# Optimization experiments

Hardware: AMD Instinct MI355X
Metric: run time of the kernel (lower is better)

The kernel has to match this reference:

```python
import jax, jax.numpy as jnp
import numpy as np
from jax import lax

K = 8          # num_classes
C_IN = 256     # in_channels
EPS = 1e-5


def resize_bilinear_ac(x, H, W):
    """Bilinear resize with align_corners=True. x: [B,C,h,w] -> [B,C,H,W]."""
    B, C, h, w = x.shape
    if h == H and w == W:
        return x
    ys = jnp.linspace(0.0, h - 1.0, H)
    xs = jnp.linspace(0.0, w - 1.0, W)
    y0 = jnp.floor(ys).astype(jnp.int32)
    x0 = jnp.floor(xs).astype(jnp.int32)
    y1 = jnp.minimum(y0 + 1, h - 1)
    x1 = jnp.minimum(x0 + 1, w - 1)
    wy = (ys - y0.astype(x.dtype))[None, None, :, None]
    wx = (xs - x0.astype(x.dtype))[None, None, None, :]
    g00 = x[:, :, y0][:, :, :, x0]
    g01 = x[:, :, y0][:, :, :, x1]
    g10 = x[:, :, y1][:, :, :, x0]
    g11 = x[:, :, y1][:, :, :, x1]
    top = g00 * (1.0 - wx) + g01 * wx
    bot = g10 * (1.0 - wx) + g11 * wx
    return top * (1.0 - wy) + bot * wy


def setup_inputs() -> dict:
    key = jax.random.key(0)
    ks = jax.random.split(key, 16)
    shapes = [(2, 256, 128, 128), (2, 256, 64, 64), (2, 256, 32, 32), (2, 256, 16, 16), (2, 256, 8, 8)]
    inp = {}
    for i, s in enumerate(shapes):
        inp[f"feat{i}"] = jax.random.normal(ks[i], s, dtype=jnp.float32)
    inp["attr_feat"] = jax.random.normal(ks[5], (2, K * C_IN, 64, 64), dtype=jnp.float32)
    # learned params
    inp["mlp_f_w"] = jax.random.normal(ks[6], (256, 256), dtype=jnp.float32) * 0.02
    inp["mlp_f_b"] = jnp.zeros((256,), dtype=jnp.float32)
    inp["mlp_a_w"] = jax.random.normal(ks[7], (256, 256), dtype=jnp.float32) * 0.02
    inp["mlp_a_b"] = jnp.zeros((256,), dtype=jnp.float32)
    # 5 grouped convs: [out=2048, in_per_group=256, 3, 3] each, no bias (BN follows)
    inp["conv_w"] = jax.random.normal(ks[8], (5, K * C_IN, C_IN, 3, 3), dtype=jnp.float32) * 0.02
    inp["bn_gamma"] = jnp.ones((5, K * C_IN), dtype=jnp.float32)
    inp["bn_beta"] = jnp.zeros((5, K * C_IN), dtype=jnp.float32)
    inp["bn_mean"] = jax.random.normal(ks[9], (5, K * C_IN), dtype=jnp.float32) * 0.1
    inp["bn_var"] = jax.random.uniform(ks[10], (5, K * C_IN), dtype=jnp.float32, minval=0.5, maxval=1.5)
    return inp


def _forward(feats, attr_feat, mlp_f_w, mlp_f_b, mlp_a_w, mlp_a_b, conv_w, bn_gamma, bn_beta, bn_mean, bn_var):
    B = attr_feat.shape[0]
    # global avg pool attr -> [B, K, C] -> mlp_a
    avg_attr = attr_feat.mean(axis=(2, 3)).reshape(B, K, C_IN)
    avg_attr = avg_attr @ mlp_a_w.T + mlp_a_b  # [B,K,256]
    outs = []
    for i, x in enumerate(feats):
        _, C, H, W = x.shape
        avg_x = x.mean(axis=(2, 3)) @ mlp_f_w.T + mlp_f_b          # [B,256]
        logits = jnp.einsum('bkc,bc->bk', avg_attr, avg_x)          # [B,K]
        attn = jax.nn.softmax(logits, axis=-1)
        y = resize_bilinear_ac(attr_feat, H, W)                      # [B,2048,H,W]
        y = lax.conv_general_dilated(
            y, conv_w[i], window_strides=(1, 1), padding=((1, 1), (1, 1)),
            dimension_numbers=('NCHW', 'OIHW', 'NCHW'), feature_group_count=K)
        inv = lax.rsqrt(bn_var[i] + EPS)
        y = (y - bn_mean[i][None, :, None, None]) * (inv * bn_gamma[i])[None, :, None, None] + bn_beta[i][None, :, None, None]
        y = jax.nn.relu(y)
        y = y.reshape(B, K, C, H, W)
        y = jnp.einsum('bkchw,bk->bchw', y, attn)                   # weighted sum over classes
        outs.append(jax.nn.relu(x + y))
    return tuple(outs)


def reference(feat0, feat1, feat2, feat3, feat4, attr_feat, mlp_f_w, mlp_f_b, mlp_a_w, mlp_a_b, conv_w, bn_gamma, bn_beta, bn_mean, bn_var):
    feats = [feat0, feat1, feat2, feat3, feat4]
    return _forward(feats, attr_feat, mlp_f_w, mlp_f_b, mlp_a_w, mlp_a_b, conv_w, bn_gamma, bn_beta, bn_mean, bn_var)
```

## Files before the change

### kernel.cpp

```cpp
#include <hip/hip_runtime.h>
#include <hip/hip_bf16.h>
#include <cstdint>

typedef __attribute__((ext_vector_type(8))) short short8;
typedef __attribute__((ext_vector_type(4))) float f32x4;

#define EPSV 1e-5f

__device__ __forceinline__ void gload_lds16(const void* g, void* l) {
  __builtin_amdgcn_global_load_lds(
      (const __attribute__((address_space(1))) void*)(uintptr_t)g,
      (__attribute__((address_space(3))) void*)(uint32_t)(uintptr_t)l,
      16, 0, 0);
}

__device__ __forceinline__ uint32_t f2bf_rne(float v) {
  const uint32_t u = __float_as_uint(v);
  const uint32_t r = ((u >> 16) & 1u) + 0x7fffu;
  return (u + r) >> 16;
}
__device__ __forceinline__ float bf2f(uint32_t u) {
  return __uint_as_float(u << 16);
}

__global__ void mean_kernel(const float* __restrict__ in, float* __restrict__ out,
                            int HW, float inv) {
  const int ch = blockIdx.x;
  const int t = threadIdx.x;
  const float* p = in + (size_t)ch * HW;
  float s = 0.f;
  const int nv = HW >> 2;
  const float4* pv = (const float4*)p;
  for (int i = t; i < nv; i += 256) { float4 v = pv[i]; s += v.x + v.y + v.z + v.w; }
  __shared__ float red[256];
  red[t] = s; __syncthreads();
  for (int off = 128; off > 0; off >>= 1) {
    if (t < off) red[t] += red[t + off];
    __syncthreads();
  }
  if (t == 0) out[ch] = red[0] * inv;
}

__global__ void meanf_kernel(const float* __restrict__ f0, const float* __restrict__ f1,
                             const float* __restrict__ f2, const float* __restrict__ f3,
                             const float* __restrict__ f4, float* __restrict__ out) {
  const int scale = blockIdx.x >> 9;
  const int ch = blockIdx.x & 511;
  const int t = threadIdx.x;
  const float* base;
  int HW;
  switch (scale) {
    case 0: base = f0; HW = 16384; break;
    case 1: base = f1; HW = 4096;  break;
    case 2: base = f2; HW = 1024;  break;
    case 3: base = f3; HW = 256;   break;
    default: base = f4; HW = 64;   break;
  }
  const float* p = base + (size_t)ch * HW;
  float s = 0.f;
  const int nv = HW >> 2;
  const float4* pv = (const float4*)p;
  for (int i = t; i < nv; i += 256) { float4 v = pv[i]; s += v.x + v.y + v.z + v.w; }
  __shared__ float red[256];
  red[t] = s; __syncthreads();
  for (int off = 128; off > 0; off >>= 1) {
    if (t < off) red[t] += red[t + off];
    __syncthreads();
  }
  if (t == 0) out[scale * 512 + ch] = red[0] / (float)HW;
}

__global__ void wtrans_kernel(const float* __restrict__ cw,
                              const float* __restrict__ gamma, const float* __restrict__ beta,
                              const float* __restrict__ mean, const float* __restrict__ var,
                              __hip_bfloat16* __restrict__ wt, float* __restrict__ bias) {
  __shared__ float wl[2304];
  const int oc = blockIdx.x;
  const int i  = blockIdx.y;
  const int t  = threadIdx.x;
  const int idx = i * 2048 + oc;
  const float* src = cw + (size_t)idx * 2304;
  for (int e = t; e < 2304; e += 256) wl[e] = src[e];
  __syncthreads();
  const float sc = rsqrtf(var[idx] + EPSV) * gamma[idx];
  if (t == 0) bias[idx] = beta[idx] - mean[idx] * sc;
  const int g = oc >> 8, co = oc & 255;
  const size_t dbase = (size_t)(i * 8 + g) * 9 * 65536 + co * 256 + t;
#pragma unroll
  for (int tap = 0; tap < 9; ++tap)
    wt[dbase + (size_t)tap * 65536] = __float2bfloat16(wl[t * 9 + tap] * sc);
}

__global__ void gate_kernel(const float* __restrict__ meanA, const float* __restrict__ meanF,
                            const float* __restrict__ Wa, const float* __restrict__ ba,
                            const float* __restrict__ Wf, const float* __restrict__ bfp,
                            float* __restrict__ attn) {
  __shared__ float mA[16 * 256];
  __shared__ float mF[10 * 256];
  __shared__ float pA[16 * 256];
  __shared__ float pF[10 * 256];
  __shared__ float lg[80];
  const int t = threadIdx.x;
  for (int i = t; i < 4096; i += 256) mA[i] = meanA[i];
  for (int i = t; i < 2560; i += 256) mF[i] = meanF[i];
  __syncthreads();
  {
    float acc[16];
#pragma unroll
    for (int j = 0; j < 16; ++j) acc[j] = 0.f;
    for (int ci = 0; ci < 256; ++ci) {
      const float w = Wa[t * 256 + ci];
#pragma unroll
      for (int j = 0; j < 16; ++j) acc[j] += mA[j * 256 + ci] * w;
    }
    const float bb = ba[t];
#pragma unroll
    for (int j = 0; j < 16; ++j) pA[j * 256 + t] = acc[j] + bb;
  }
  {
    float acc[10];
#pragma unroll
    for (int j = 0; j < 10; ++j) acc[j] = 0.f;
    for (int ci = 0; ci < 256; ++ci) {
      const float w = Wf[t * 256 + ci];
#pragma unroll
      for (int j = 0; j < 10; ++j) acc[j] += mF[j * 256 + ci] * w;
    }
    const float bb = bfp[t];
#pragma unroll
    for (int j = 0; j < 10; ++j) pF[j * 256 + t] = acc[j] + bb;
  }
  __syncthreads();
  if (t < 80) {
    const int i = t >> 4, r = t & 15, b = r >> 3, k = r & 7;
    const float* a = &pA[(b * 8 + k) * 256];
    const float* f = &pF[(i * 2 + b) * 256];
    float d = 0.f;
    for (int c = 0; c < 256; ++c) d += a[c] * f[c];
    lg[t] = d;
  }
  __syncthreads();
  if (t < 10) {
    const int base = t * 8;
    float m = lg[base];
    for (int k = 1; k < 8; ++k) m = fmaxf(m, lg[base + k]);
    float e[8], s = 0.f;
    for (int k = 0; k < 8; ++k) { e[k] = __expf(lg[base + k] - m); s += e[k]; }
    const float invs = 1.f / s;
    for (int k = 0; k < 8; ++k) attn[base + k] = e[k] * invs;
  }
}

__global__ void resize_kernel(const float* __restrict__ attr,
                              __hip_bfloat16* __restrict__ R,
                              int W, int Hp, int Wp, float scl) {
  const int bk = blockIdx.x;
  const int yp = blockIdx.y;
  const int t  = threadIdx.x;
  const size_t rowbase = ((size_t)bk * Hp + yp) * (size_t)Wp * 256;
  if (yp == 0 || yp == Hp - 1) {
    uint32_t* p = (uint32_t*)(R + rowbase);
    const int n = Wp * 128;
    for (int idx = t; idx < n; idx += 256) p[idx] = 0u;
    return;
  }
  const int y = yp - 1;
  const float fy = y * scl;
  int y0 = (int)floorf(fy); if (y0 > 63) y0 = 63;
  const float wy = fy - (float)y0;
  const int y1 = min(y0 + 1, 63);
  __shared__ float buf[2][64][65];
  const int cc = t >> 2, seg = (t & 3) * 16;
  const int bb = bk >> 3, k = bk & 7;
  const float* ab = attr + (size_t)bb * 2048 * 4096;
  const int ci = t & 63;
  for (int cq = 0; cq < 4; ++cq) {
    __syncthreads();
    {
      const int ch = k * 256 + cq * 64 + cc;
      const float* r0 = ab + ((size_t)ch * 64 + y0) * 64;
      const float* r1 = ab + ((size_t)ch * 64 + y1) * 64;
#pragma unroll
      for (int u = 0; u < 4; ++u) {
        float4 v0 = ((const float4*)r0)[(t & 3) * 4 + u];
        float4 v1 = ((const float4*)r1)[(t & 3) * 4 + u];
        buf[0][cc][seg + u * 4 + 0] = v0.x; buf[0][cc][seg + u * 4 + 1] = v0.y;
        buf[0][cc][seg + u * 4 + 2] = v0.z; buf[0][cc][seg + u * 4 + 3] = v0.w;
        buf[1][cc][seg + u * 4 + 0] = v1.x; buf[1][cc][seg + u * 4 + 1] = v1.y;
        buf[1][cc][seg + u * 4 + 2] = v1.z; buf[1][cc][seg + u * 4 + 3] = v1.w;
      }
    }
    __syncthreads();
    for (int x = t >> 6; x < W; x += 4) {
      const float fx = x * scl;
      int x0 = (int)floorf(fx); if (x0 > 63) x0 = 63;
      const float wx = fx - (float)x0;
      const int x1 = min(x0 + 1, 63);
      const float top = buf[0][ci][x0] * (1.f - wx) + buf[0][ci][x1] * wx;
      const float bot = buf[1][ci][x0] * (1.f - wx) + buf[1][ci][x1] * wx;
      R[rowbase + (size_t)(x + 1) * 256 + cq * 64 + ci] = __float2bfloat16(top * (1.f - wy) + bot * wy);
    }
    if (t < 64) {
      R[rowbase + cq * 64 + t] = __float2bfloat16(0.f);
      R[rowbase + (size_t)(Wp - 1) * 256 + cq * 64 + t] = __float2bfloat16(0.f);
    }
  }
}

__device__ __forceinline__ void coords36(int u, int g0, int& g, int& ty, int& tx, int& cq) {
  g = g0 + u / 36;
  const int r = u % 36;
  const int tap = r >> 2;
  cq = r & 3;
  ty = tap / 3;
  tx = tap - ty * 3;
}

__global__ __launch_bounds__(512, 1)
void conv256_kernel(const __hip_bfloat16* __restrict__ R,
                    const __hip_bfloat16* __restrict__ Wt,
                    const float* __restrict__ bias,
                    const float* __restrict__ attn,
                    __hip_bfloat16* __restrict__ zout,
                    int W, int lw, int Hp, int Wp, int HW,
                    int NB, int gcount) {
  __shared__ alignas(16) __hip_bfloat16 ldsA[2][256 * 64];
  __shared__ alignas(16) __hip_bfloat16 ldsB[2][256 * 64];
  const int tid  = threadIdx.x;
  const int lane = tid & 63;
  const int wave = __builtin_amdgcn_readfirstlane(tid >> 6);
  const int wm = (wave >> 2) * 128;
  const int wn = (wave & 3) * 64;

  const int X = gridDim.x;
  int xp = blockIdx.x, yv = blockIdx.y;
  if (X * gridDim.y == 256) {
    const int lin2 = blockIdx.x + X * blockIdx.y;
    const int d = (lin2 & 7) * 32 + (lin2 >> 3);
    yv = d / X; xp = d - yv * X;
  }
  const int n0 = xp * 256;
  const int bb = yv % NB;
  const int gs = yv / NB;
  const int g0 = gs * gcount;

  const int c8 = lane & 7, r8 = lane >> 3;
  const int sc = (c8 ^ r8) << 3;
  const int aoff0 = ((wave * 32 + r8) << 8) + sc;
  const int dst0  = wave * 2048;
  int boff[4];
#pragma unroll
  for (int q = 0; q < 4; ++q) {
    const int row = wave * 32 + q * 8 + r8;
    const int sg = n0 + row;
    const int y = sg >> lw, x = sg & (W - 1);
    boff[q] = ((y * Wp + x) << 8) + sc;
  }

  const size_t rgstride = (size_t)Hp * Wp * 256;
  const __hip_bfloat16* Rb = R + (size_t)bb * 8 * rgstride;

  const f32x4 fz = {0.f, 0.f, 0.f, 0.f};
  f32x4 acc[8][4];
  uint32_t finp[8][4][2];
#pragma unroll
  for (int mf = 0; mf < 8; ++mf)
#pragma unroll
    for (int nf = 0; nf < 4; ++nf) {
      acc[mf][nf] = fz; finp[mf][nf][0] = 0u; finp[mf][nf][1] = 0u;
    }

  const int nk = gcount * 36;
  {
    const __hip_bfloat16* wp = Wt + ((size_t)g0 * 9 << 16);
    const __hip_bfloat16* rp = Rb + (size_t)g0 * rgstride;
#pragma unroll
    for (int q = 0; q < 4; ++q) gload_lds16(wp + aoff0 + q * 2048, &ldsA[0][dst0 + q * 512]);
#pragma unroll
    for (int q = 0; q < 4; ++q) gload_lds16(rp + boff[q], &ldsB[0][dst0 + q * 512]);
  }

  int foldc = 0, gcur = g0;
  for (int t = 0; t < nk; ++t) {
    const int c = t & 1;
    const bool pf = (t + 1 < nk);
    int g1, ty1, tx1, cq1;
    coords36(pf ? t + 1 : t, g0, g1, ty1, tx1, cq1);
    const __hip_bfloat16* wp1 = Wt + (((size_t)g1 * 9 + ty1 * 3 + tx1) << 16) + (cq1 << 6);
    const __hip_bfloat16* rp1 = Rb + (size_t)g1 * rgstride + ((ty1 * Wp + tx1) << 8) + (cq1 << 6);

    asm volatile("s_waitcnt vmcnt(0)" ::: "memory");
    __builtin_amdgcn_s_barrier();
    asm volatile("" ::: "memory");

    const __hip_bfloat16* pA = &ldsA[c][0];
    const __hip_bfloat16* pB = &ldsB[c][0];
    __hip_bfloat16* dA = &ldsA[c ^ 1][0];
    __hip_bfloat16* dB = &ldsB[c ^ 1][0];

#pragma unroll
    for (int ks = 0; ks < 2; ++ks) {
      const int cb = ks * 4 + (lane >> 4);
      short8 bfv[4];
#pragma unroll
      for (int nf = 0; nf < 4; ++nf) {
        const int row = wn + nf * 16 + (lane & 15);
        bfv[nf] = *(const short8*)&pB[(row << 6) + ((cb ^ (row & 7)) << 3)];
      }
#pragma unroll
      for (int h = 0; h < 2; ++h) {
        short8 af[4];
#pragma unroll
        for (int m = 0; m < 4; ++m) {
          const int row = wm + (h * 4 + m) * 16 + (lane & 15);
          af[m] = *(const short8*)&pA[(row << 6) + ((cb ^ (row & 7)) << 3)];
        }
        if (ks == 0 && pf) {
          if (h == 0) {
#pragma unroll
            for (int q = 0; q < 4; ++q) gload_lds16(wp1 + aoff0 + q * 2048, dA + dst0 + q * 512);
          } else {
#pragma unroll
            for (int q = 0; q < 4; ++q) gload_lds16(rp1 + boff[q], dB + dst0 + q * 512);
          }
        }
        __builtin_amdgcn_s_barrier();
        __builtin_amdgcn_sched_barrier(0);
        __builtin_amdgcn_s_setprio(1);
#pragma unroll
        for (int m = 0; m < 4; ++m)
#pragma unroll
          for (int nf = 0; nf < 4; ++nf)
            acc[h * 4 + m][nf] = __builtin_amdgcn_mfma_f32_16x16x32_bf16(
                af[m], bfv[nf], acc[h * 4 + m][nf], 0, 0, 0);
        __builtin_amdgcn_s_setprio(0);
        __builtin_amdgcn_s_barrier();
        asm volatile("" ::: "memory");
      }
    }

    if (++foldc == 36) {
      foldc = 0;
      const float aw = attn[bb * 8 + gcur];
#pragma unroll
      for (int mf = 0; mf < 8; ++mf) {
        const int cobase = wm + mf * 16 + ((lane >> 4) << 2);
#pragma unroll
        for (int pr = 0; pr < 2; ++pr) {
          const float b0v = bias[(gcur << 8) + cobase + pr * 2 + 0];
          const float b1v = bias[(gcur << 8) + cobase + pr * 2 + 1];
#pragma unroll
          for (int nf = 0; nf < 4; ++nf) {
            const uint32_t p = finp[mf][nf][pr];
            const float f0 = __uint_as_float(p << 16)
                           + aw * fmaxf(acc[mf][nf][pr * 2 + 0] + b0v, 0.f);
            const float f1 = __uint_as_float(p & 0xffff0000u)
                           + aw * fmaxf(acc[mf][nf][pr * 2 + 1] + b1v, 0.f);
            finp[mf][nf][pr] = (f2bf_rne(f1) << 16) | f2bf_rne(f0);
          }
        }
#pragma unroll
        for (int nf = 0; nf < 4; ++nf) acc[mf][nf] = fz;
      }
      ++gcur;
    }
  }

  __hip_bfloat16* zb = zout + (size_t)(gs * 2 + bb) * 256 * (size_t)HW;
#pragma unroll
  for (int mf = 0; mf < 8; ++mf) {
    const int cobase = wm + mf * 16 + ((lane >> 4) << 2);
#pragma unroll
    for (int nf = 0; nf < 4; ++nf) {
      const int n = n0 + wn + nf * 16 + (lane & 15);
#pragma unroll
      for (int pr = 0; pr < 2; ++pr) {
        const uint32_t p = finp[mf][nf][pr];
        zb[(size_t)(cobase + pr * 2 + 0) * HW + n] =
            __float2bfloat16(__uint_as_float(p << 16));
        zb[(size_t)(cobase + pr * 2 + 1) * HW + n] =
            __float2bfloat16(__uint_as_float(p & 0xffff0000u));
      }
    }
  }
}

__global__ __launch_bounds__(256, 2)
void conv_kernel(const __hip_bfloat16* __restrict__ R,
                 const __hip_bfloat16* __restrict__ Wt,
                 const float* __restrict__ bias,
                 const float* __restrict__ attn,
                 const float* __restrict__ featp,
                 void* __restrict__ outp,
                 int W, int lw, int Hp, int Wp, int HW,
                 int b0, int NB, int gcount) {
  __shared__ alignas(16) __hip_bfloat16 ldsA[2][128 * 64];
  __shared__ alignas(16) __hip_bfloat16 ldsB[3][128 * 64];
  const int tid  = threadIdx.x;
  const int lane = tid & 63;
  const int wave = __builtin_amdgcn_readfirstlane(tid >> 6);
  const int wm = (wave >> 1) * 64;
  const int wn = (wave & 1) * 64;

  const int nx  = gridDim.x;
  const int lin = blockIdx.x;
  const int pos = ((nx & 7) == 0) ? ((lin & 7) * (nx >> 3) + (lin >> 3)) : lin;
  const int co0 = (pos & 1) * 128;
  const int n0  = (pos >> 1) * 128;

  const int bb  = (int)blockIdx.y % NB;
  const int gs  = (int)blockIdx.y / NB;
  const int b   = b0 + bb;
  const int g0  = gs * gcount;

  const int c8 = lane & 7;
  const int r8 = lane >> 3;
  int aoff[4], boff[4], dst[4];
#pragma unroll
  for (int q = 0; q < 4; ++q) {
    const int row = (wave * 4 + q) * 8 + r8;
    const int sc = (c8 ^ (row & 7)) << 3;
    aoff[q] = ((co0 + row) << 8) + sc;
    int sg = n0 + row; if (sg >= HW) sg = HW - 1;
    const int y = sg >> lw, x = sg & (W - 1);
    boff[q] = ((y * Wp + x) << 8) + sc;
    dst[q] = (wave * 4 + q) * 512;
  }

  const size_t rgstride = (size_t)Hp * Wp * 256;
  const __hip_bfloat16* Rb = R + (size_t)bb * 8 * rgstride;

  const f32x4 fz = {0.f, 0.f, 0.f, 0.f};
  f32x4 fin[4][4], acc[4][4];
#pragma unroll
  for (int mf = 0; mf < 4; ++mf)
#pragma unroll
    for (int nf = 0; nf < 4; ++nf) { fin[mf][nf] = fz; acc[mf][nf] = fz; }

  const int nstages = gcount * 36;
  {
    int g, ty, tx, cq;
    coords36(0, g0, g, ty, tx, cq);
    const __hip_bfloat16* wp = Wt + (((size_t)g * 9 + ty * 3 + tx) << 16) + (cq << 6);
    const __hip_bfloat16* rp = Rb + (size_t)g * rgstride + ((ty * Wp + tx) << 8) + (cq << 6);
#pragma unroll
    for (int q = 0; q < 4; ++q) gload_lds16(wp + aoff[q], &ldsA[0][dst[q]]);
#pragma unroll
    for (int q = 0; q < 4; ++q) gload_lds16(rp + boff[q], &ldsB[0][dst[q]]);
    coords36(1 < nstages ? 1 : 0, g0, g, ty, tx, cq);
    const __hip_bfloat16* rp1 = Rb + (size_t)g * rgstride + ((ty * Wp + tx) << 8) + (cq << 6);
#pragma unroll
    for (int q = 0; q < 4; ++q) gload_lds16(rp1 + boff[q], &ldsB[1][dst[q]]);
  }

  int bcur = 0, b2 = 2;
  int foldc = 0, gcur = g0;

  for (int s = 0; s < nstages; ++s) {
    __builtin_amdgcn_s_barrier();
    asm volatile("" ::: "memory");
    if (s + 1 < nstages) {
      int g, ty, tx, cq;
      coords36(s + 1, g0, g, ty, tx, cq);
      const __hip_bfloat16* wp = Wt + (((size_t)g * 9 + ty * 3 + tx) << 16) + (cq << 6);
      __hip_bfloat16* dA = &ldsA[(s + 1) & 1][0];
#pragma unroll
      for (int q = 0; q < 4; ++q) gload_lds16(wp + aoff[q], dA + dst[q]);
    }
    if (s + 2 < nstages) {
      int g, ty, tx, cq;
      coords36(s + 2, g0, g, ty, tx, cq);
      const __hip_bfloat16* rp = Rb + (size_t)g * rgstride + ((ty * Wp + tx) << 8) + (cq << 6);
      __hip_bfloat16* dB = &ldsB[b2][0];
#pragma unroll
      for (int q = 0; q < 4; ++q) gload_lds16(rp + boff[q], dB + dst[q]);
    }
    if (s + 2 < nstages)      asm volatile("s_waitcnt vmcnt(12)" ::: "memory");
    else if (s + 1 < nstages) asm volatile("s_waitcnt vmcnt(8)" ::: "memory");
    else                      asm volatile("s_waitcnt vmcnt(0)" ::: "memory");
    __builtin_amdgcn_s_barrier();
    asm volatile("" ::: "memory");

    const __hip_bfloat16* pA = &ldsA[s & 1][0];
    const __hip_bfloat16* pB = &ldsB[bcur][0];
#pragma unroll
    for (int ks = 0; ks < 2; ++ks) {
      short8 af[4], bfv[4];
      const int cb = ks * 4 + (lane >> 4);
#pragma unroll
      for (int mf = 0; mf < 4; ++mf) {
        const int row = wm + mf * 16 + (lane & 15);
        af[mf] = *(const short8*)&pA[(row << 6) + ((cb ^ (row & 7)) << 3)];
      }
#pragma unroll
      for (int nf = 0; nf < 4; ++nf) {
        const int row = wn + nf * 16 + (lane & 15);
        bfv[nf] = *(const short8*)&pB[(row << 6) + ((cb ^ (row & 7)) << 3)];
      }
#pragma unroll
      for (int mf = 0; mf < 4; ++mf)
#pragma unroll
        for (int nf = 0; nf < 4; ++nf)
          acc[mf][nf] = __builtin_amdgcn_mfma_f32_16x16x32_bf16(
              af[mf], bfv[nf], acc[mf][nf], 0, 0, 0);
    }

    if (++bcur == 3) bcur = 0;
    if (++b2 == 3) b2 = 0;

    if (++foldc == 36) {
      foldc = 0;
      const float aw = attn[b * 8 + gcur];
#pragma unroll
      for (int mf = 0; mf < 4; ++mf) {
        const int cobase = co0 + wm + mf * 16 + ((lane >> 4) << 2);
#pragma unroll
        for (int r = 0; r < 4; ++r) {
          const float bs = bias[(gcur << 8) + cobase + r];
#pragma unroll
          for (int nf = 0; nf < 4; ++nf) {
            fin[mf][nf][r] += aw * fmaxf(acc[mf][nf][r] + bs, 0.f);
            acc[mf][nf][r] = 0.f;
          }
        }
      }
      ++gcur;
    }
  }

  const size_t plane = (size_t)256 * HW;
  if (featp) {
    const float* fb = featp + (size_t)b * plane;
    float* ob = (float*)outp + (size_t)b * plane;
#pragma unroll
    for (int mf = 0; mf < 4; ++mf) {
      const int cobase = co0 + wm + mf * 16 + ((lane >> 4) << 2);
#pragma unroll
      for (int nf = 0; nf < 4; ++nf) {
        const int n = n0 + wn + nf * 16 + (lane & 15);
        if (n < HW) {
#pragma unroll
          for (int r = 0; r < 4; ++r) {
            const size_t idx = (size_t)(cobase + r) * HW + n;
            ob[idx] = fmaxf(fb[idx] + fin[mf][nf][r], 0.f);
          }
        }
      }
    }
  } else {
    __hip_bfloat16* zb = (__hip_bfloat16*)outp + ((size_t)gs * 2 + b) * plane;
#pragma unroll
    for (int mf = 0; mf < 4; ++mf) {
      const int cobase = co0 + wm + mf * 16 + ((lane >> 4) << 2);
#pragma unroll
      for (int nf = 0; nf < 4; ++nf) {
        const int n = n0 + wn + nf * 16 + (lane & 15);
        if (n < HW) {
#pragma unroll
          for (int r = 0; r < 4; ++r)
            zb[(size_t)(cobase + r) * HW + n] = __float2bfloat16(fin[mf][nf][r]);
        }
      }
    }
  }
}

__global__ void reduce_kernel(const __hip_bfloat16* __restrict__ z,
                              const float* __restrict__ feat,
                              float* __restrict__ outp, int total, int S) {
  const int i4 = (blockIdx.x * 256 + threadIdx.x) * 4;
  if (i4 >= total) return;
  float4 f = *(const float4*)(feat + i4);
  float s0 = f.x, s1 = f.y, s2 = f.z, s3 = f.w;
  for (int j = 0; j < S; ++j) {
    const ushort4 v = *(const ushort4*)(z + (size_t)j * total + i4);
    s0 += bf2f(v.x);
    s1 += bf2f(v.y);
    s2 += bf2f(v.z);
    s3 += bf2f(v.w);
  }
  float4 o = {fmaxf(s0, 0.f), fmaxf(s1, 0.f), fmaxf(s2, 0.f), fmaxf(s3, 0.f)};
  *(float4*)(outp + i4) = o;
}

extern "C" void kernel_launch(void* const* d_in, const int* in_sizes, int n_in,
                              void* d_out, int out_size, void* d_ws, size_t ws_size,
                              hipStream_t stream) {
  const float* feat[5];
  for (int i = 0; i < 5; ++i) feat[i] = (const float*)d_in[i];
  const float* attr = (const float*)d_in[5];
  const float* mfw = (const float*)d_in[6];
  const float* mfb = (const float*)d_in[7];
  const float* maw = (const float*)d_in[8];
  const float* mab = (const float*)d_in[9];
  const float* cw  = (const float*)d_in[10];
  const float* bng = (const float*)d_in[11];
  const float* bnb = (const float*)d_in[12];
  const float* bnm = (const float*)d_in[13];
  const float* bnv = (const float*)d_in[14];
  float* out = (float*)d_out;

  char* ws = (char*)d_ws;
  float* attnW = (float*)(ws);
  float* meanA = (float*)(ws + 512);
  float* meanF = (float*)(ws + 20480);
  float* biasW = (float*)(ws + 32768);
  __hip_bfloat16* Wt = (__hip_bfloat16*)(ws + 131072);
  const size_t R_OFF = 47316992;
  __hip_bfloat16* Rbuf = (__hip_bfloat16*)(ws + R_OFF);

  const bool full = ws_size >= (size_t)219316224;
  const int NB = full ? 2 : 1;
  __hip_bfloat16* zbuf = (__hip_bfloat16*)(ws + R_OFF + (size_t)NB * 69222400);

  static const int HS[5] = {128, 64, 32, 16, 8};
  static const size_t OOFF[5] = {0, 8388608, 10485760, 11010048, 11141120};

  mean_kernel<<<4096, 256, 0, stream>>>(attr, meanA, 4096, 1.f / 4096.f);
  meanf_kernel<<<2560, 256, 0, stream>>>(feat[0], feat[1], feat[2], feat[3], feat[4], meanF);
  wtrans_kernel<<<dim3(2048, 5), 256, 0, stream>>>(cw, bng, bnb, bnm, bnv, Wt, biasW);
  gate_kernel<<<1, 256, 0, stream>>>(meanA, meanF, maw, mab, mfw, mfb, attnW);

  for (int i = 0; i < 5; ++i) {
    const int H = HS[i], W = H, HW = H * W, Hp = H + 2, Wp = W + 2;
    const int lw = 31 - __builtin_clz((unsigned)W);
    const float scl = 63.f / (float)(H - 1);

    if (full) {
      resize_kernel<<<dim3(16, Hp), 256, 0, stream>>>(attr, Rbuf, W, Hp, Wp, scl);
      if (i <= 1) {
        const int S = (i == 0) ? 2 : 8;
        const int gcount = 8 / S;
        conv256_kernel<<<dim3(HW / 256, 2 * S), 512, 0, stream>>>(
            Rbuf, Wt + (size_t)i * 8 * 9 * 65536, biasW + i * 2048, attnW + i * 16,
            zbuf, W, lw, Hp, Wp, HW, 2, gcount);
        const int total = 2 * 256 * HW;
        reduce_kernel<<<(total / 4 + 255) / 256, 256, 0, stream>>>(
            zbuf, feat[i], out + OOFF[i], total, S);
      } else {
        const int ntiles = (HW + 127) / 128;
        conv_kernel<<<dim3(ntiles * 2, 2 * 8), 256, 0, stream>>>(
            Rbuf, Wt + (size_t)i * 8 * 9 * 65536, biasW + i * 2048, attnW + i * 16,
            nullptr, zbuf, W, lw, Hp, Wp, HW, 0, 2, 1);
        const int total = 2 * 256 * HW;
        reduce_kernel<<<(total / 4 + 255) / 256, 256, 0, stream>>>(
            zbuf, feat[i], out + OOFF[i], total, 8);
      }
    } else {
      const int ntiles = (HW + 127) / 128;
      for (int b0 = 0; b0 < 2; ++b0) {
        resize_kernel<<<dim3(8, Hp), 256, 0, stream>>>(
            attr + (size_t)b0 * 2048 * 4096, Rbuf, W, Hp, Wp, scl);
        conv_kernel<<<dim3(ntiles * 2, 1), 256, 0, stream>>>(
            Rbuf, Wt + (size_t)i * 8 * 9 * 65536, biasW + i * 2048, attnW + i * 16,
            feat[i], out + OOFF[i], W, lw, Hp, Wp, HW, b0, 1, 8);
      }
    }
  }
}
```

Before: 724.8 us.

## Reuse 64x64 bf16 padded resize as source for other scales, per-scale weight transform

Processes scale 1 (64x64, same size as attr) first, storing a padded bf16 NHWC copy of attr. The other scales then bilinearly resample from that compact bf16 buffer instead of re-reading the fp32 NCHW attr tensor, which cuts global traffic for the resize kernels. Weight transform now runs per scale into a single reused buffer, shrinking the workspace. The trade-off is extra bf16 rounding: the resized values are interpolated from already-rounded bf16 values, so they carry slightly more error.

Result: faster. 706.6 us, median of 2 (-2.5%).

```diff
diff --git a/kernel.cpp b/kernel.cpp
--- a/kernel.cpp
+++ b/kernel.cpp
@@ -73,10 +73,10 @@
 __global__ void wtrans_kernel(const float* __restrict__ cw,
                               const float* __restrict__ gamma, const float* __restrict__ beta,
                               const float* __restrict__ mean, const float* __restrict__ var,
-                              __hip_bfloat16* __restrict__ wt, float* __restrict__ bias) {
+                              __hip_bfloat16* __restrict__ wt, float* __restrict__ bias,
+                              int i) {
   __shared__ float wl[2304];
   const int oc = blockIdx.x;
-  const int i  = blockIdx.y;
   const int t  = threadIdx.x;
   const int idx = i * 2048 + oc;
   const float* src = cw + (size_t)idx * 2304;
@@ -85,7 +85,7 @@
   const float sc = rsqrtf(var[idx] + EPSV) * gamma[idx];
   if (t == 0) bias[idx] = beta[idx] - mean[idx] * sc;
   const int g = oc >> 8, co = oc & 255;
-  const size_t dbase = (size_t)(i * 8 + g) * 9 * 65536 + co * 256 + t;
+  const size_t dbase = (size_t)g * 9 * 65536 + co * 256 + t;
 #pragma unroll
   for (int tap = 0; tap < 9; ++tap)
     wt[dbase + (size_t)tap * 65536] = __float2bfloat16(wl[t * 9 + tap] * sc);
@@ -207,6 +207,60 @@
   }
 }
 
+__global__ void resizeR1_kernel(const __hip_bfloat16* __restrict__ R1,
+                                __hip_bfloat16* __restrict__ R,
+                                int W, int Hp, int Wp, float scl) {
+  const int bk = blockIdx.x;
+  const int yp = blockIdx.y;
+  const int t  = threadIdx.x;
+  const size_t rowbase = ((size_t)bk * Hp + yp) * (size_t)Wp * 256;
+  if (yp == 0 || yp == Hp - 1) {
+    uint32_t* p = (uint32_t*)(R + rowbase);
+    const int n = Wp * 128;
+    for (int idx = t; idx < n; idx += 256) p[idx] = 0u;
+    return;
+  }
+  const int y = yp - 1;
+  const float fy = y * scl;
+  int y0 = (int)floorf(fy); if (y0 > 63) y0 = 63;
+  const float wy = fy - (float)y0;
+  const int y1 = min(y0 + 1, 63);
+  const __hip_bfloat16* r0 = R1 + ((size_t)bk * 66 + (y0 + 1)) * 66 * 256 + 256;
+  const __hip_bfloat16* r1 = R1 + ((size_t)bk * 66 + (y1 + 1)) * 66 * 256 + 256;
+  const int ci4 = (t & 63) * 4;
+  for (int x = t >> 6; x < W; x += 4) {
+    const float fx = x * scl;
+    int x0 = (int)floorf(fx); if (x0 > 63) x0 = 63;
+    const float wx = fx - (float)x0;
+    const int x1 = min(x0 + 1, 63);
+    const ushort4 a00 = *(const ushort4*)&r0[x0 * 256 + ci4];
+    const ushort4 a01 = *(const ushort4*)&r0[x1 * 256 + ci4];
+    const ushort4 a10 = *(const ushort4*)&r1[x0 * 256 + ci4];
+    const ushort4 a11 = *(const ushort4*)&r1[x1 * 256 + ci4];
+    short4 st;
+    {
+      const float t0 = bf2f(a00.x) * (1.f - wx) + bf2f(a01.x) * wx;
+      const float b0 = bf2f(a10.x) * (1.f - wx) + bf2f(a11.x) * wx;
+      st.x = (short)f2bf_rne(t0 * (1.f - wy) + b0 * wy);
+      const float t1 = bf2f(a00.y) * (1.f - wx) + bf2f(a01.y) * wx;
+      const float b1 = bf2f(a10.y) * (1.f - wx) + bf2f(a11.y) * wx;
+      st.y = (short)f2bf_rne(t1 * (1.f - wy) + b1 * wy);
+      const float t2 = bf2f(a00.z) * (1.f - wx) + bf2f(a01.z) * wx;
+      const float b2 = bf2f(a10.z) * (1.f - wx) + bf2f(a11.z) * wx;
+      st.z = (short)f2bf_rne(t2 * (1.f - wy) + b2 * wy);
+      const float t3 = bf2f(a00.w) * (1.f - wx) + bf2f(a01.w) * wx;
+      const float b3 = bf2f(a10.w) * (1.f - wx) + bf2f(a11.w) * wx;
+      st.w = (short)f2bf_rne(t3 * (1.f - wy) + b3 * wy);
+    }
+    *(short4*)&R[rowbase + (size_t)(x + 1) * 256 + ci4] = st;
+  }
+  if (t < 64) {
+    const short4 z4 = {0, 0, 0, 0};
+    *(short4*)&R[rowbase + t * 4] = z4;
+    *(short4*)&R[rowbase + (size_t)(Wp - 1) * 256 + t * 4] = z4;
+  }
+}
+
 __device__ __forceinline__ void coords36(int u, int g0, int& g, int& ty, int& tx, int& cq) {
   g = g0 + u / 36;
   const int r = u % 36;
@@ -605,54 +659,67 @@
   float* meanA = (float*)(ws + 512);
   float* meanF = (float*)(ws + 20480);
   float* biasW = (float*)(ws + 32768);
-  __hip_bfloat16* Wt = (__hip_bfloat16*)(ws + 131072);
-  const size_t R_OFF = 47316992;
-  __hip_bfloat16* Rbuf = (__hip_bfloat16*)(ws + R_OFF);
-
-  const bool full = ws_size >= (size_t)219316224;
-  const int NB = full ? 2 : 1;
-  __hip_bfloat16* zbuf = (__hip_bfloat16*)(ws + R_OFF + (size_t)NB * 69222400);
+  __hip_bfloat16* Wt  = (__hip_bfloat16*)(ws + 131072);
+  __hip_bfloat16* R1  = (__hip_bfloat16*)(ws + 9568256);
+  __hip_bfloat16* R0  = (__hip_bfloat16*)(ws + 45252608);
+  __hip_bfloat16* zbuf = (__hip_bfloat16*)(ws + 183697408);
+
+  const bool full = ws_size >= (size_t)217251840;
 
   static const int HS[5] = {128, 64, 32, 16, 8};
   static const size_t OOFF[5] = {0, 8388608, 10485760, 11010048, 11141120};
+  static const int ORDER[5] = {1, 0, 2, 3, 4};
 
   mean_kernel<<<4096, 256, 0, stream>>>(attr, meanA, 4096, 1.f / 4096.f);
   meanf_kernel<<<2560, 256, 0, stream>>>(feat[0], feat[1], feat[2], feat[3], feat[4], meanF);
-  wtrans_kernel<<<dim3(2048, 5), 256, 0, stream>>>(cw, bng, bnb, bnm, bnv, Wt, biasW);
   gate_kernel<<<1, 256, 0, stream>>>(meanA, meanF, maw, mab, mfw, mfb, attnW);
 
-  for (int i = 0; i < 5; ++i) {
-    const int H = HS[i], W = H, HW = H * W, Hp = H + 2, Wp = W + 2;
-    const int lw = 31 - __builtin_clz((unsigned)W);
-    const float scl = 63.f / (float)(H - 1);
-
-    if (full) {
-      resize_kernel<<<dim3(16, Hp), 256, 0, stream>>>(attr, Rbuf, W, Hp, Wp, scl);
+  if (full) {
+    for (int oi = 0; oi < 5; ++oi) {
+      const int i = ORDER[oi];
+      const int H = HS[i], W = H, HW = H * W, Hp = H + 2, Wp = W + 2;
+      const int lw = 31 - __builtin_clz((unsigned)W);
+      const float scl = 63.f / (float)(H - 1);
+      __hip_bfloat16* Ri = (i == 1) ? R1 : R0;
+
+      wtrans_kernel<<<2048, 256, 0, stream>>>(cw, bng, bnb, bnm, bnv, Wt, biasW, i);
+      if (i == 1)
+        resize_kernel<<<dim3(16, Hp), 256, 0, stream>>>(attr, R1, W, Hp, Wp, scl);
+      else
+        resizeR1_kernel<<<dim3(16, Hp), 256, 0, stream>>>(R1, Ri, W, Hp, Wp, scl);
+
       if (i <= 1) {
         const int S = (i == 0) ? 2 : 8;
         const int gcount = 8 / S;
         conv256_kernel<<<dim3(HW / 256, 2 * S), 512, 0, stream>>>(
-            Rbuf, Wt + (size_t)i * 8 * 9 * 65536, biasW + i * 2048, attnW + i * 16,
+            Ri, Wt, biasW + i * 2048, attnW + i * 16,
             zbuf, W, lw, Hp, Wp, HW, 2, gcount);
         const int total = 2 * 256 * HW;
         reduce_kernel<<<(total / 4 + 255) / 256, 256, 0, stream>>>(
             zbuf, feat[i], out + OOFF[i], total, S);
       } else {
         const int ntiles = (HW + 127) / 128;
-        conv_kernel<<<dim3(ntiles * 2, 2 * 8), 256, 0, stream>>>(
-            Rbuf, Wt + (size_t)i * 8 * 9 * 65536, biasW + i * 2048, attnW + i * 16,
+        conv_kernel<<<dim3(ntiles * 2, 16), 256, 0, stream>>>(
+            Ri, Wt, biasW + i * 2048, attnW + i * 16,
             nullptr, zbuf, W, lw, Hp, Wp, HW, 0, 2, 1);
         const int total = 2 * 256 * HW;
         reduce_kernel<<<(total / 4 + 255) / 256, 256, 0, stream>>>(
             zbuf, feat[i], out + OOFF[i], total, 8);
       }
-    } else {
+    }
+  } else {
+    __hip_bfloat16* Rbuf = R1;
+    for (int i = 0; i < 5; ++i) {
+      const int H = HS[i], W = H, HW = H * W, Hp = H + 2, Wp = W + 2;
+      const int lw = 31 - __builtin_clz((unsigned)W);
+      const float scl = 63.f / (float)(H - 1);
+      wtrans_kernel<<<2048, 256, 0, stream>>>(cw, bng, bnb, bnm, bnv, Wt, biasW, i);
       const int ntiles = (HW + 127) / 128;
       for (int b0 = 0; b0 < 2; ++b0) {
         resize_kernel<<<dim3(8, Hp), 256, 0, stream>>>(
             attr + (size_t)b0 * 2048 * 4096, Rbuf, W, Hp, Wp, scl);
         conv_kernel<<<dim3(ntiles * 2, 1), 256, 0, stream>>>(
-            Rbuf, Wt + (size_t)i * 8 * 9 * 65536, biasW + i * 2048, attnW + i * 16,
+            Rbuf, Wt, biasW + i * 2048, attnW + i * 16,
             feat[i], out + OOFF[i], W, lw, Hp, Wp, HW, b0, 1, 8);
       }
     }
```
